# Performance work log

Hardware: AMD Instinct MI355X
Metric: run time of the kernel (lower is better)

## Reference

```python
import jax, jax.numpy as jnp
import numpy as np

B, N, SU, H, NC, NUM_ITER = 1024, 32, 8, 64, 4, 5
E = N * (N - 1)


def _edge_idx(n):
    # Fully-connected graph without self loops; edges grouped contiguously by
    # destination node so that blocks of (n-1) messages sum into one node
    # (matches the original Python segment-sum loop with step = n-1).
    idx = np.arange(n)
    temp_a = np.concatenate([np.delete(idx, j) for j in range(n)])  # sources
    temp_b = np.repeat(idx, n - 1)                                   # destinations
    return temp_a, temp_b


def _lin(x, W, b):
    return x @ W.T + b


def setup_inputs():
    key = jax.random.key(0)
    ks = jax.random.split(key, 20)
    f = jax.random.normal
    return {
        "read_gru": f(ks[0], (B, N, SU), jnp.float32),
        "gru_init": f(ks[1], (B, N, H), jnp.float32),
        "init_features": f(ks[2], (B, N, 3), jnp.float32),
        "edge_weight": f(ks[3], (B, E), jnp.float32),
        "noise_info": jax.random.uniform(ks[4], (B, 1), jnp.float32),
        "x_hat_EP": f(ks[5], (B, N), jnp.float32),
        "variance_EP": jax.random.uniform(ks[6], (B, N), jnp.float32),
        "W1a": f(ks[7], (SU, 3)) * 0.3, "b1a": jnp.zeros((SU,)),
        "W2a": f(ks[8], (H, 2 * SU + 2)) * 0.1, "b2a": jnp.zeros((H,)),
        "W2b": f(ks[9], (H // 2, H)) * 0.1, "b2b": jnp.zeros((H // 2,)),
        "W2c": f(ks[10], (SU, H // 2)) * 0.1, "b2c": jnp.zeros((SU,)),
        "Wih": f(ks[11], (3 * H, SU + 2)) * 0.1, "bih": jnp.zeros((3 * H,)),
        "Whh": f(ks[12], (3 * H, H)) * 0.1, "bhh": jnp.zeros((3 * H,)),
        "W3a": f(ks[13], (H, SU)) * 0.1, "b3a": jnp.zeros((H,)),
        "W3b": f(ks[14], (H // 2, H)) * 0.1, "b3b": jnp.zeros((H // 2,)),
        "W3c": f(ks[15], (NC, H // 2)) * 0.1, "b3c": jnp.zeros((NC,)),
        "W4": f(ks[16], (SU, H)) * 0.1, "b4": jnp.zeros((SU,)),
        "GNN_iter": 0,
    }


def reference(read_gru, gru_init, init_features, edge_weight, noise_info,
              x_hat_EP, variance_EP,
              W1a, b1a, W2a, b2a, W2b, b2b, W2c, b2c,
              Wih, bih, Whh, bhh,
              W3a, b3a, W3b, b3b, W3c, b3c, W4, b4, GNN_iter):
    b, n = init_features.shape[0], init_features.shape[1]
    temp_a, temp_b = _edge_idx(n)
    e = temp_a.shape[0]
    edge_e = edge_weight[:, :, None]                              # [B,E,1]
    noise_e = jnp.broadcast_to(noise_info, (b, e))[:, :, None]    # [B,E,1]
    gru_hidden = gru_init
    for it in range(NUM_ITER):
        if it == 0 and GNN_iter == 0:
            init_nodes = _lin(init_features, W1a, b1a)            # [B,N,SU]
        else:
            init_nodes = read_gru
        s1 = init_nodes[:, temp_a, :]                             # gather sources
        s2 = init_nodes[:, temp_b, :]                             # gather dests
        comb = jnp.concatenate([s1, s2, edge_e, noise_e], axis=2) # [B,E,2SU+2]
        m = jax.nn.relu(_lin(comb, W2a, b2a))
        m = jax.nn.relu(_lin(m, W2b, b2b))
        m = jax.nn.relu(_lin(m, W2c, b2c))                        # [B,E,SU]
        # contiguous blocks of (n-1) messages per destination node
        sum_msgs = m.reshape(b, n, n - 1, -1).sum(axis=2)         # [B,N,SU]
        gin = jnp.concatenate(
            [sum_msgs, x_hat_EP[:, :, None], variance_EP[:, :, None]], axis=2)
        # GRUCell applied per node
        gi = _lin(gin, Wih, bih)
        gh = _lin(gru_hidden, Whh, bhh)
        i_r, i_z, i_n = jnp.split(gi, 3, axis=-1)
        h_r, h_z, h_n = jnp.split(gh, 3, axis=-1)
        r = jax.nn.sigmoid(i_r + h_r)
        z = jax.nn.sigmoid(i_z + h_z)
        cand = jnp.tanh(i_n + r * h_n)
        gru_hidden = (1.0 - z) * cand + z * gru_hidden
        read_gru = _lin(gru_hidden, W4, b4)
    # readout (no activations in original forward)
    p_y_x = _lin(_lin(_lin(read_gru, W3a, b3a), W3b, b3b), W3c, b3c)
    return (p_y_x, read_gru, gru_hidden)
```

## Files before the change

### kernel.cpp

```cpp
#include <hip/hip_runtime.h>
#include <hip/hip_bf16.h>

#define BB 1024
#define NN 32
#define SUD 8
#define HD 64
#define NCD 4
#define ED 992
#define NITER 5

#define O_W2AT 0
#define O_B2A  1152
#define O_W2B  1216
#define O_B2B  3264
#define O_W2CT 3296
#define O_B2C  3552
#define O_WIHT 3560
#define O_BIH  5480
#define O_WHHT 5672
#define O_BHH  17960
#define O_W4T  18152
#define O_B4   18664
#define O_W3AT 18672
#define O_B3A  19184
#define O_W3BT 19248
#define O_B3B  21296
#define O_W3CT 21328
#define O_B3C  21456
#define O_W1AT 21460
#define O_B1A  21484
#define W_TOTAL 21492

#define FRAG_B2_HI  0
#define FRAG_B2_LO  2048
#define FRAG_C      4096
#define FRAG_WHH_HI 4608
#define FRAG_WHH_LO 16896
#define W_EXT (W_TOTAL + 2560 + 12288)

#define GHS 196

typedef const float* fwp;
typedef __attribute__((ext_vector_type(8))) short short8;
typedef __attribute__((ext_vector_type(4))) float float4v;

__device__ __forceinline__ short bf16r(float x) {
  __hip_bfloat16 h = __float2bfloat16(x);
  return __builtin_bit_cast(short, h);
}

__global__ void prep_weights(fwp W2a, fwp b2a, fwp W2b, fwp b2b, fwp W2c, fwp b2c,
                             fwp Wih, fwp bih, fwp Whh, fwp bhh,
                             fwp W3a, fwp b3a, fwp W3b, fwp b3b, fwp W3c, fwp b3c,
                             fwp W4, fwp b4, fwp W1a, fwp b1a, float* __restrict__ ws) {
  int idx = blockIdx.x * 256 + threadIdx.x;
  if (idx >= W_EXT) return;
  if (idx >= W_TOTAL) {
    __hip_bfloat16* wb = (__hip_bfloat16*)(ws + W_TOTAL);
    int e = idx - W_TOTAL;
    if (e < 2048) {
      int j = e & 7, L = (e >> 3) & 63, hs = e >> 9;
      int h = hs >> 1, s = hs & 1;
      float v = W2b[(h * 16 + (L & 15)) * 64 + s * 32 + ((L >> 4) & 3) * 8 + j];
      float hi = __bfloat162float(__float2bfloat16(v));
      wb[FRAG_B2_HI + e] = __float2bfloat16(v);
      wb[FRAG_B2_LO + e] = __float2bfloat16(v - hi);
    } else if (e < 2560) {
      int e2 = e - 2048;
      int j = e2 & 7, L = (e2 >> 3) & 63;
      int su = L & 15, q = L >> 4;
      float v = (su < 8) ? W2c[su * 32 + q * 8 + j] : 0.f;
      wb[FRAG_C + e2] = __float2bfloat16(v);
    } else {
      int e2 = e - 2560;
      int j = e2 & 7, L = (e2 >> 3) & 63, nts = e2 >> 9;
      int nt = nts >> 1, s = nts & 1;
      float v = Whh[(nt * 16 + (L & 15)) * 64 + s * 32 + ((L >> 4) & 3) * 8 + j];
      float hi = __bfloat162float(__float2bfloat16(v));
      wb[FRAG_WHH_HI + e2] = __float2bfloat16(v);
      wb[FRAG_WHH_LO + e2] = __float2bfloat16(v - hi);
    }
    return;
  }
  float v;
  if (idx < O_B2A)       { int p = idx;          int su = p / 64, f = p % 64;   v = W2a[f * 18 + su]; }
  else if (idx < O_W2B)  { v = b2a[idx - O_B2A]; }
  else if (idx < O_B2B)  { v = W2b[idx - O_W2B]; }
  else if (idx < O_W2CT) { v = b2b[idx - O_B2B]; }
  else if (idx < O_B2C)  { int p = idx - O_W2CT; int o = p / 8, su = p % 8;     v = W2c[su * 32 + o]; }
  else if (idx < O_WIHT) { v = b2c[idx - O_B2C]; }
  else if (idx < O_BIH)  { int p = idx - O_WIHT; int k = p / 192, o = p % 192;  v = Wih[o * 10 + k]; }
  else if (idx < O_WHHT) { v = bih[idx - O_BIH]; }
  else if (idx < O_BHH)  { int p = idx - O_WHHT; int k = p / 192, o = p % 192;  v = Whh[o * 64 + k]; }
  else if (idx < O_W4T)  { v = bhh[idx - O_BHH]; }
  else if (idx < O_B4)   { int p = idx - O_W4T;  int k = p / 8, su = p % 8;     v = W4[su * 64 + k]; }
  else if (idx < O_W3AT) { v = b4[idx - O_B4]; }
  else if (idx < O_B3A)  { int p = idx - O_W3AT; int k = p / 64, f = p % 64;    v = W3a[f * 8 + k]; }
  else if (idx < O_W3BT) { v = b3a[idx - O_B3A]; }
  else if (idx < O_B3B)  { int p = idx - O_W3BT; int k = p / 32, f = p % 32;    v = W3b[f * 64 + k]; }
  else if (idx < O_W3CT) { v = b3b[idx - O_B3B]; }
  else if (idx < O_B3C)  { int p = idx - O_W3CT; int k = p / 4, c = p % 4;      v = W3c[c * 32 + k]; }
  else if (idx < O_W1AT) { v = b3c[idx - O_B3C]; }
  else if (idx < O_B1A)  { int p = idx - O_W1AT; int c = p / 8, su = p % 8;     v = W1a[su * 3 + c]; }
  else                   { v = b1a[idx - O_B1A]; }
  ws[idx] = v;
}

#define DO_STEP(KOFF, Y0, Y1, W0, W1, FH0, FH1)                                \
  {                                                                            \
    float4v x0 = *(const float4v*)&sA1[a * 68 + (KOFF)];                       \
    float4v x1 = *(const float4v*)&sA1[a * 68 + (KOFF) + 4];                   \
    float4v z4 = {0.f, 0.f, 0.f, 0.f};                                         \
    float4v t0 = (x0 + Y0) + ewv * W0;                                         \
    float4v t1 = (x1 + Y1) + ewv * W1;                                         \
    t0 = __builtin_elementwise_max(t0, z4);                                    \
    t1 = __builtin_elementwise_max(t1, z4);                                    \
    short8 ahi;                                                                \
    ahi[0] = bf16r(t0.x); ahi[1] = bf16r(t0.y); ahi[2] = bf16r(t0.z);          \
    ahi[3] = bf16r(t0.w); ahi[4] = bf16r(t1.x); ahi[5] = bf16r(t1.y);          \
    ahi[6] = bf16r(t1.z); ahi[7] = bf16r(t1.w);                                \
    accb0 = __builtin_amdgcn_mfma_f32_16x16x32_bf16(ahi, FH0, accb0, 0, 0, 0); \
    accb1 = __builtin_amdgcn_mfma_f32_16x16x32_bf16(ahi, FH1, accb1, 0, 0, 0); \
  }

#define LAUNDER(v) __asm__ __volatile__("" : "+v"(v))

__global__ __launch_bounds__(256, 4) void gnn_fused(
    const float* __restrict__ read_gru_in,
    const float* __restrict__ gru_init,
    const float* __restrict__ feat,
    const float* __restrict__ edge_w,
    const float* __restrict__ noise_in,
    const float* __restrict__ xhat,
    const float* __restrict__ vep,
    const int* __restrict__ gnn_iter_p,
    const float* __restrict__ ws,
    float* __restrict__ out)
{
  __shared__ __attribute__((aligned(16))) char spool[NN * GHS * 4];
  __shared__ __attribute__((aligned(16))) float sH[NN * 68];
  __shared__ float sNodes[NN * 9];
  __shared__ float sSum[NN * 8];
  __shared__ float sEw[ED];
  __shared__ float sC1[64];
  __shared__ float sWew[64];
  __shared__ float sX[NN];
  __shared__ float sV[NN];

  float* const sA1 = (float*)spool;
  float* const sA2 = (float*)(spool + 8704);
  __hip_bfloat16* const sM2 = (__hip_bfloat16*)(spool + 17408);
  float* const sGH = (float*)spool;

  const int b = blockIdx.x;
  const int t = threadIdx.x;
  const int lane = t & 63;
  const int wv = t >> 6;
  const int quad = lane >> 4;
  const int lm = lane & 15;

  const __hip_bfloat16* wb = (const __hip_bfloat16*)(ws + W_TOTAL);

  float noi = noise_in[b];
  for (int e = t; e < ED; e += 256) sEw[e] = edge_w[b * ED + e];
  if (t < NN) { sX[t] = xhat[b * NN + t]; sV[t] = vep[b * NN + t]; }
  if (t < 64) {
    sC1[t]  = ws[O_B2A + t] + noi * ws[O_W2AT + 17 * 64 + t];
    sWew[t] = ws[O_W2AT + 16 * 64 + t];
  }
#pragma unroll
  for (int i = 0; i < 8; ++i) {
    int p = t + 256 * i;
    sH[(p >> 6) * 68 + (p & 63)] = gru_init[b * (NN * HD) + p];
  }
  {
    const int git = gnn_iter_p[0];
    int n = t >> 3, su = t & 7;
    float acc;
    if (git == 0) {
      acc = ws[O_B1A + su];
#pragma unroll
      for (int c = 0; c < 3; ++c)
        acc += ws[O_W1AT + c * 8 + su] * feat[b * (NN * 3) + n * 3 + c];
    } else {
      acc = read_gru_in[b * (NN * SUD) + t];
    }
    sNodes[n * 9 + su] = acc;
  }
  __syncthreads();

  for (int it = 0; it < NITER; ++it) {
    {
      int iva = 0; LAUNDER(iva);
      const float* wsl = ws + iva;
#pragma unroll
      for (int i = 0; i < 8; ++i) {
        int p = t + 256 * i;
        int n = p >> 6, f = p & 63;
        float a1 = 0.f, a2 = 0.f;
#pragma unroll
        for (int su = 0; su < 8; ++su) {
          float nv = sNodes[n * 9 + su];
          a1 += wsl[O_W2AT + su * 64 + f] * nv;
          a2 += wsl[O_W2AT + (8 + su) * 64 + f] * nv;
        }
        sA1[n * 68 + f] = a1;
        sA2[n * 68 + f] = a2 + sC1[iva + f];
      }
    }
    __syncthreads();

    {
      int ive = 0; LAUNDER(ive);
      const float* wsl = ws + ive;
      const __hip_bfloat16* wbl = wb + ive;
      short8 fbh00 = *(const short8*)(wbl + FRAG_B2_HI + (0 * 64 + lane) * 8);
      short8 fbh01 = *(const short8*)(wbl + FRAG_B2_HI + (1 * 64 + lane) * 8);
      short8 fbh10 = *(const short8*)(wbl + FRAG_B2_HI + (2 * 64 + lane) * 8);
      short8 fbh11 = *(const short8*)(wbl + FRAG_B2_HI + (3 * 64 + lane) * 8);
      short8 fcf   = *(const short8*)(wbl + FRAG_C + lane * 8);
      const float b2b0 = wsl[O_B2B + lm];
      const float b2b1 = wsl[O_B2B + 16 + lm];
      const float b2cl = wsl[O_B2C + lm];

      __hip_bfloat16* m2w = sM2 + wv * (16 * 44);
      const int kq0 = quad * 8, kq1 = 32 + quad * 8;
      float4v wwA = *(const float4v*)&sWew[ive + kq0];
      float4v wwB = *(const float4v*)&sWew[ive + kq0 + 4];
      float4v wwC = *(const float4v*)&sWew[ive + kq1];
      float4v wwD = *(const float4v*)&sWew[ive + kq1 + 4];
      for (int ni = 0; ni < 8; ++ni) {
        const int jj = wv * 8 + ni;
        float4v yA = *(const float4v*)&sA2[jj * 68 + kq0];
        float4v yB = *(const float4v*)&sA2[jj * 68 + kq0 + 4];
        float4v yC = *(const float4v*)&sA2[jj * 68 + kq1];
        float4v yD = *(const float4v*)&sA2[jj * 68 + kq1 + 4];
        float psum = 0.f;
#pragma unroll
        for (int tile = 0; tile < 2; ++tile) {
          int kk = tile * 16 + lm;
          int kk2 = (kk < 31) ? kk : 0;
          int a = kk2 + (kk2 >= jj ? 1 : 0);
          float ewv = (kk < 31) ? sEw[ive + jj * 31 + kk] : 0.f;
          float4v accb0 = {0.f, 0.f, 0.f, 0.f};
          float4v accb1 = {0.f, 0.f, 0.f, 0.f};
          DO_STEP(kq0, yA, yB, wwA, wwB, fbh00, fbh10);
          DO_STEP(kq1, yC, yD, wwC, wwD, fbh01, fbh11);
#pragma unroll
          for (int r = 0; r < 4; ++r) {
            float m20 = fmaxf(accb0[r] + b2b0, 0.f);
            float m21 = fmaxf(accb1[r] + b2b1, 0.f);
            m2w[(quad * 4 + r) * 44 + lm]      = __float2bfloat16(m20);
            m2w[(quad * 4 + r) * 44 + 16 + lm] = __float2bfloat16(m21);
          }
          __asm__ __volatile__("" ::: "memory");
          short8 ac = *(const short8*)(m2w + lm * 44 + quad * 8);
          float4v c3 = {0.f, 0.f, 0.f, 0.f};
          c3 = __builtin_amdgcn_mfma_f32_16x16x32_bf16(ac, fcf, c3, 0, 0, 0);
#pragma unroll
          for (int r = 0; r < 4; ++r) {
            float v = fmaxf(c3[r] + b2cl, 0.f);
            if (tile == 1 && r == 3) v = (quad == 3) ? 0.f : v;
            psum += v;
          }
          __asm__ __volatile__("" ::: "memory");
        }
        psum += __shfl_xor(psum, 16);
        psum += __shfl_xor(psum, 32);
        if (lane < 8) sSum[jj * 8 + lane] = psum;
      }
    }
    __syncthreads();

    {
      int ivg = 0; LAUNDER(ivg);
      const __hip_bfloat16* wbl = wb + ivg;
      short8 aH[2][2];
#pragma unroll
      for (int mt = 0; mt < 2; ++mt) {
#pragma unroll
        for (int s = 0; s < 2; ++s) {
          const float* hp = &sH[(mt * 16 + lm) * 68 + s * 32 + quad * 8];
          float4v h0 = *(const float4v*)hp;
          float4v h1 = *(const float4v*)(hp + 4);
          short8 a;
          a[0] = bf16r(h0.x); a[1] = bf16r(h0.y); a[2] = bf16r(h0.z); a[3] = bf16r(h0.w);
          a[4] = bf16r(h1.x); a[5] = bf16r(h1.y); a[6] = bf16r(h1.z); a[7] = bf16r(h1.w);
          aH[mt][s] = a;
        }
      }
#pragma unroll
      for (int nt = 0; nt < 3; ++nt) {
        int gnt = 4 * nt + wv;
        short8 bh0 = *(const short8*)(wbl + FRAG_WHH_HI + ((gnt * 2 + 0) * 64 + lane) * 8);
        short8 bh1 = *(const short8*)(wbl + FRAG_WHH_HI + ((gnt * 2 + 1) * 64 + lane) * 8);
#pragma unroll
        for (int mt = 0; mt < 2; ++mt) {
          float4v acc = {0.f, 0.f, 0.f, 0.f};
          acc = __builtin_amdgcn_mfma_f32_16x16x32_bf16(aH[mt][0], bh0, acc, 0, 0, 0);
          acc = __builtin_amdgcn_mfma_f32_16x16x32_bf16(aH[mt][1], bh1, acc, 0, 0, 0);
#pragma unroll
          for (int r = 0; r < 4; ++r)
            sGH[(mt * 16 + quad * 4 + r) * GHS + gnt * 16 + lm] = acc[r];
        }
      }
    }
    __asm__ __volatile__("" ::: "memory");

    {
      int ivq = 0; LAUNDER(ivq);
      const float* wsl = ws + ivq;
      int lm2 = lane & 15, g = lane >> 4;
      int c = wv * 16 + lm2;
      float ar[8], az[8], inx[8];
      {
        float br  = wsl[O_BIH + c]       + wsl[O_BHH + c];
        float bz  = wsl[O_BIH + 64 + c]  + wsl[O_BHH + 64 + c];
        float bni = wsl[O_BIH + 128 + c];
#pragma unroll
        for (int j = 0; j < 8; ++j) { ar[j] = br; az[j] = bz; inx[j] = bni; }
      }
#pragma unroll
      for (int k = 0; k < 8; ++k) {
        float wr = wsl[O_WIHT + k * 192 + c];
        float wz = wsl[O_WIHT + k * 192 + 64 + c];
        float wn = wsl[O_WIHT + k * 192 + 128 + c];
#pragma unroll
        for (int j = 0; j < 8; ++j) {
          float gg = sSum[(g + 4 * j) * 8 + k];
          ar[j] += wr * gg; az[j] += wz * gg; inx[j] += wn * gg;
        }
      }
      {
        float wr = wsl[O_WIHT + 8 * 192 + c];
        float wz = wsl[O_WIHT + 8 * 192 + 64 + c];
        float wn = wsl[O_WIHT + 8 * 192 + 128 + c];
#pragma unroll
        for (int j = 0; j < 8; ++j) {
          float gg = sX[ivq + g + 4 * j];
          ar[j] += wr * gg; az[j] += wz * gg; inx[j] += wn * gg;
        }
        wr = wsl[O_WIHT + 9 * 192 + c];
        wz = wsl[O_WIHT + 9 * 192 + 64 + c];
        wn = wsl[O_WIHT + 9 * 192 + 128 + c];
#pragma unroll
        for (int j = 0; j < 8; ++j) {
          float gg = sV[ivq + g + 4 * j];
          ar[j] += wr * gg; az[j] += wz * gg; inx[j] += wn * gg;
        }
      }
      float bnh = wsl[O_BHH + 128 + c];
      float hnew[8];
#pragma unroll
      for (int j = 0; j < 8; ++j) {
        int n = g + 4 * j;
        float ghr = sGH[n * GHS + c];
        float ghz = sGH[n * GHS + 64 + c];
        float ghn = sGH[n * GHS + 128 + c] + bnh;
        float r = 1.f / (1.f + __expf(-(ar[j] + ghr)));
        float z = 1.f / (1.f + __expf(-(az[j] + ghz)));
        float cd = inx[j] + r * ghn;
        float e2 = __expf(2.f * cd);
        float th = 1.f - 2.f / (e2 + 1.f);
        hnew[j] = (1.f - z) * th + z * sH[n * 68 + c];
      }
      __syncthreads();
#pragma unroll
      for (int j = 0; j < 8; ++j) sH[(g + 4 * j) * 68 + c] = hnew[j];
    }
    __syncthreads();

    {
      int ivw = 0; LAUNDER(ivw);
      const float* wsl = ws + ivw;
      int n = t >> 3, su = t & 7;
      float c0 = 0.f, c1v = 0.f, c2 = 0.f, c3v = 0.f;
#pragma unroll
      for (int k = 0; k < 64; k += 4) {
        c0  += wsl[O_W4T + (k + 0) * 8 + su] * sH[n * 68 + k + 0];
        c1v += wsl[O_W4T + (k + 1) * 8 + su] * sH[n * 68 + k + 1];
        c2  += wsl[O_W4T + (k + 2) * 8 + su] * sH[n * 68 + k + 2];
        c3v += wsl[O_W4T + (k + 3) * 8 + su] * sH[n * 68 + k + 3];
      }
      sNodes[n * 9 + su] = wsl[O_B4 + su] + ((c0 + c1v) + (c2 + c3v));
    }
    __syncthreads();
  }

#pragma unroll
  for (int i = 0; i < 8; ++i) {
    int p = t + 256 * i;
    int n = p >> 6, f = p & 63;
    float acc = ws[O_B3A + f];
#pragma unroll
    for (int k = 0; k < 8; ++k) acc += ws[O_W3AT + k * 64 + f] * sNodes[n * 9 + k];
    sA1[n * 68 + f] = acc;
  }
  __syncthreads();
#pragma unroll
  for (int i = 0; i < 4; ++i) {
    int p = t + 256 * i;
    int n = p >> 5, f = p & 31;
    float c0 = 0.f, c1v = 0.f, c2 = 0.f, c3v = 0.f;
#pragma unroll
    for (int k = 0; k < 64; k += 4) {
      c0  += ws[O_W3BT + (k + 0) * 32 + f] * sA1[n * 68 + k + 0];
      c1v += ws[O_W3BT + (k + 1) * 32 + f] * sA1[n * 68 + k + 1];
      c2  += ws[O_W3BT + (k + 2) * 32 + f] * sA1[n * 68 + k + 2];
      c3v += ws[O_W3BT + (k + 3) * 32 + f] * sA1[n * 68 + k + 3];
    }
    sA2[n * 33 + f] = ws[O_B3B + f] + ((c0 + c1v) + (c2 + c3v));
  }
  __syncthreads();
  if (t < 128) {
    int n = t >> 2, c = t & 3;
    float acc = ws[O_B3C + c];
#pragma unroll
    for (int k = 0; k < 32; ++k) acc += ws[O_W3CT + k * 4 + c] * sA2[n * 33 + k];
    out[b * (NN * NCD) + t] = acc;
  }
  out[BB * NN * NCD + b * (NN * SUD) + t] = sNodes[(t >> 3) * 9 + (t & 7)];
#pragma unroll
  for (int i = 0; i < 8; ++i) {
    int p = t + 256 * i;
    out[BB * NN * NCD + BB * NN * SUD + b * (NN * HD) + p] =
        sH[(p >> 6) * 68 + (p & 63)];
  }
}

extern "C" void kernel_launch(void* const* d_in, const int* in_sizes, int n_in,
                              void* d_out, int out_size, void* d_ws, size_t ws_size,
                              hipStream_t stream) {
  typedef const float* F32;
  F32 read_gru = (F32)d_in[0];
  F32 gru_init = (F32)d_in[1];
  F32 feat     = (F32)d_in[2];
  F32 edge_w   = (F32)d_in[3];
  F32 noise    = (F32)d_in[4];
  F32 xh       = (F32)d_in[5];
  F32 vp       = (F32)d_in[6];
  F32 W1a = (F32)d_in[7];  F32 b1a = (F32)d_in[8];
  F32 W2a = (F32)d_in[9];  F32 b2a = (F32)d_in[10];
  F32 W2b = (F32)d_in[11]; F32 b2b = (F32)d_in[12];
  F32 W2c = (F32)d_in[13]; F32 b2c = (F32)d_in[14];
  F32 Wih = (F32)d_in[15]; F32 bih = (F32)d_in[16];
  F32 Whh = (F32)d_in[17]; F32 bhh = (F32)d_in[18];
  F32 W3a = (F32)d_in[19]; F32 b3a = (F32)d_in[20];
  F32 W3b = (F32)d_in[21]; F32 b3b = (F32)d_in[22];
  F32 W3c = (F32)d_in[23]; F32 b3c = (F32)d_in[24];
  F32 W4  = (F32)d_in[25]; F32 b4  = (F32)d_in[26];
  const int* git = (const int*)d_in[27];
  float* ws = (float*)d_ws;

  prep_weights<<<(W_EXT + 255) / 256, 256, 0, stream>>>(
      W2a, b2a, W2b, b2b, W2c, b2c, Wih, bih, Whh, bhh,
      W3a, b3a, W3b, b3b, W3c, b3c, W4, b4, W1a, b1a, ws);

  gnn_fused<<<BB, 256, 0, stream>>>(read_gru, gru_init, feat, edge_w, noise,
                                    xh, vp, git, ws, (float*)d_out);
}
```

Baseline: 267.5 us.

## Move node projection to MFMA, hoist fragment loads, pack GRU input math

The per-iteration W2a node projection now runs on bf16 MFMA instead of scalar FMAs, using new pre-swizzled fragments built in prep. The W2b/W2c fragments and biases are hoisted out of the iteration loop, and the unused hi/lo split buffers are dropped. The W2b layout is interleaved so bias loads and message stores can be packed pairs. The GRU input projection uses float2 packed math over a new interleaved Wih copy, and the W4 readout reads raw W4 with float4 vector loads. This trades some precision in the node projection (bf16 inputs) for fewer VALU instructions, and the hoisted fragments raise register pressure.

```diff
diff --git a/kernel.cpp b/kernel.cpp
--- a/kernel.cpp
+++ b/kernel.cpp
@@ -30,23 +30,29 @@
 #define O_W1AT 21460
 #define O_B1A  21484
 #define W_TOTAL 21492
-
-#define FRAG_B2_HI  0
-#define FRAG_B2_LO  2048
-#define FRAG_C      4096
-#define FRAG_WHH_HI 4608
-#define FRAG_WHH_LO 16896
-#define W_EXT (W_TOTAL + 2560 + 12288)
+#define O_WIHP 21492
+#define W_TOTAL2 25332
+
+#define FRAG_B2   0
+#define FRAG_C    2048
+#define FRAG_WHH  2560
+#define FRAG_A2P  14848
+#define FRAG_TOTAL 18944
+#define PREP_TOTAL (W_TOTAL2 + FRAG_TOTAL)
 
 #define GHS 196
 
 typedef const float* fwp;
 typedef __attribute__((ext_vector_type(8))) short short8;
 typedef __attribute__((ext_vector_type(4))) float float4v;
+typedef __attribute__((ext_vector_type(2))) float float2v;
 
 __device__ __forceinline__ short bf16r(float x) {
   __hip_bfloat16 h = __float2bfloat16(x);
   return __builtin_bit_cast(short, h);
+}
+__device__ __forceinline__ float2v mk2(float a, float b) {
+  float2v r; r.x = a; r.y = b; return r;
 }
 
 __global__ void prep_weights(fwp W2a, fwp b2a, fwp W2b, fwp b2b, fwp W2c, fwp b2c,
@@ -54,32 +60,40 @@
                              fwp W3a, fwp b3a, fwp W3b, fwp b3b, fwp W3c, fwp b3c,
                              fwp W4, fwp b4, fwp W1a, fwp b1a, float* __restrict__ ws) {
   int idx = blockIdx.x * 256 + threadIdx.x;
-  if (idx >= W_EXT) return;
-  if (idx >= W_TOTAL) {
-    __hip_bfloat16* wb = (__hip_bfloat16*)(ws + W_TOTAL);
-    int e = idx - W_TOTAL;
+  if (idx >= PREP_TOTAL) return;
+  if (idx >= W_TOTAL2) {
+    __hip_bfloat16* wbw = (__hip_bfloat16*)(ws + W_TOTAL2);
+    int e = idx - W_TOTAL2;
+    float v;
     if (e < 2048) {
       int j = e & 7, L = (e >> 3) & 63, hs = e >> 9;
       int h = hs >> 1, s = hs & 1;
-      float v = W2b[(h * 16 + (L & 15)) * 64 + s * 32 + ((L >> 4) & 3) * 8 + j];
-      float hi = __bfloat162float(__float2bfloat16(v));
-      wb[FRAG_B2_HI + e] = __float2bfloat16(v);
-      wb[FRAG_B2_LO + e] = __float2bfloat16(v - hi);
+      v = W2b[(2 * (L & 15) + h) * 64 + s * 32 + ((L >> 4) & 3) * 8 + j];
     } else if (e < 2560) {
       int e2 = e - 2048;
       int j = e2 & 7, L = (e2 >> 3) & 63;
       int su = L & 15, q = L >> 4;
-      float v = (su < 8) ? W2c[su * 32 + q * 8 + j] : 0.f;
-      wb[FRAG_C + e2] = __float2bfloat16(v);
-    } else {
+      v = (su < 8) ? W2c[su * 32 + q * 8 + j] : 0.f;
+    } else if (e < 14848) {
       int e2 = e - 2560;
       int j = e2 & 7, L = (e2 >> 3) & 63, nts = e2 >> 9;
       int nt = nts >> 1, s = nts & 1;
-      float v = Whh[(nt * 16 + (L & 15)) * 64 + s * 32 + ((L >> 4) & 3) * 8 + j];
-      float hi = __bfloat162float(__float2bfloat16(v));
-      wb[FRAG_WHH_HI + e2] = __float2bfloat16(v);
-      wb[FRAG_WHH_LO + e2] = __float2bfloat16(v - hi);
-    }
+      v = Whh[(nt * 16 + (L & 15)) * 64 + s * 32 + ((L >> 4) & 3) * 8 + j];
+    } else {
+      int e2 = e - 14848;
+      int j = e2 & 7, L = (e2 >> 3) & 63, nt = e2 >> 9;
+      int col = L & 15, kq = L >> 4;
+      v = 0.f;
+      if (kq == 0) v = (nt < 4) ? W2a[(nt * 16 + col) * 18 + j]
+                                : W2a[((nt - 4) * 16 + col) * 18 + 8 + j];
+    }
+    wbw[e] = __float2bfloat16(v);
+    return;
+  }
+  if (idx >= W_TOTAL) {
+    int p = idx - O_WIHP;
+    int o = p / 20, k = (p % 20) >> 1;
+    ws[idx] = Wih[o * 10 + k];
     return;
   }
   float v;
@@ -135,11 +149,12 @@
     const float* __restrict__ vep,
     const int* __restrict__ gnn_iter_p,
     const float* __restrict__ ws,
+    const float* __restrict__ W4g,
     float* __restrict__ out)
 {
   __shared__ __attribute__((aligned(16))) char spool[NN * GHS * 4];
   __shared__ __attribute__((aligned(16))) float sH[NN * 68];
-  __shared__ float sNodes[NN * 9];
+  __shared__ __attribute__((aligned(16))) float sNodes[NN * 10];
   __shared__ float sSum[NN * 8];
   __shared__ float sEw[ED];
   __shared__ float sC1[64];
@@ -159,7 +174,7 @@
   const int quad = lane >> 4;
   const int lm = lane & 15;
 
-  const __hip_bfloat16* wb = (const __hip_bfloat16*)(ws + W_TOTAL);
+  const __hip_bfloat16* wb = (const __hip_bfloat16*)(ws + W_TOTAL2);
 
   float noi = noise_in[b];
   for (int e = t; e < ED; e += 256) sEw[e] = edge_w[b * ED + e];
@@ -185,44 +200,57 @@
     } else {
       acc = read_gru_in[b * (NN * SUD) + t];
     }
-    sNodes[n * 9 + su] = acc;
-  }
+    sNodes[n * 10 + su] = acc;
+  }
+
+  short8 fbh00 = *(const short8*)(wb + FRAG_B2 + (0 * 64 + lane) * 8);
+  short8 fbh01 = *(const short8*)(wb + FRAG_B2 + (1 * 64 + lane) * 8);
+  short8 fbh10 = *(const short8*)(wb + FRAG_B2 + (2 * 64 + lane) * 8);
+  short8 fbh11 = *(const short8*)(wb + FRAG_B2 + (3 * 64 + lane) * 8);
+  short8 fcf   = *(const short8*)(wb + FRAG_C + lane * 8);
+  float2v b2bv = *(const float2v*)&ws[O_B2B + 2 * lm];
+  float   b2cl = ws[O_B2C + lm];
+
   __syncthreads();
 
   for (int it = 0; it < NITER; ++it) {
     {
       int iva = 0; LAUNDER(iva);
-      const float* wsl = ws + iva;
-#pragma unroll
-      for (int i = 0; i < 8; ++i) {
-        int p = t + 256 * i;
-        int n = p >> 6, f = p & 63;
-        float a1 = 0.f, a2 = 0.f;
-#pragma unroll
-        for (int su = 0; su < 8; ++su) {
-          float nv = sNodes[n * 9 + su];
-          a1 += wsl[O_W2AT + su * 64 + f] * nv;
-          a2 += wsl[O_W2AT + (8 + su) * 64 + f] * nv;
-        }
-        sA1[n * 68 + f] = a1;
-        sA2[n * 68 + f] = a2 + sC1[iva + f];
+      const __hip_bfloat16* fp = wb + FRAG_A2P + iva;
+      short8 aN[2];
+#pragma unroll
+      for (int mt = 0; mt < 2; ++mt) {
+        short8 a = {0, 0, 0, 0, 0, 0, 0, 0};
+        if (quad == 0) {
+          float4v n0 = *(const float4v*)&sNodes[(mt * 16 + lm) * 10];
+          float4v n1 = *(const float4v*)&sNodes[(mt * 16 + lm) * 10 + 4];
+          a[0] = bf16r(n0.x); a[1] = bf16r(n0.y); a[2] = bf16r(n0.z); a[3] = bf16r(n0.w);
+          a[4] = bf16r(n1.x); a[5] = bf16r(n1.y); a[6] = bf16r(n1.z); a[7] = bf16r(n1.w);
+        }
+        aN[mt] = a;
+      }
+      const int f = wv * 16 + lm;
+      const float c1f = sC1[f];
+#pragma unroll
+      for (int half = 0; half < 2; ++half) {
+        short8 bfr = *(const short8*)(fp + ((half * 4 + wv) * 64 + lane) * 8);
+#pragma unroll
+        for (int mt = 0; mt < 2; ++mt) {
+          float4v acc = {0.f, 0.f, 0.f, 0.f};
+          acc = __builtin_amdgcn_mfma_f32_16x16x32_bf16(aN[mt], bfr, acc, 0, 0, 0);
+#pragma unroll
+          for (int r = 0; r < 4; ++r) {
+            int node = mt * 16 + quad * 4 + r;
+            if (half == 0) sA1[node * 68 + f] = acc[r];
+            else           sA2[node * 68 + f] = acc[r] + c1f;
+          }
+        }
       }
     }
     __syncthreads();
 
     {
       int ive = 0; LAUNDER(ive);
-      const float* wsl = ws + ive;
-      const __hip_bfloat16* wbl = wb + ive;
-      short8 fbh00 = *(const short8*)(wbl + FRAG_B2_HI + (0 * 64 + lane) * 8);
-      short8 fbh01 = *(const short8*)(wbl + FRAG_B2_HI + (1 * 64 + lane) * 8);
-      short8 fbh10 = *(const short8*)(wbl + FRAG_B2_HI + (2 * 64 + lane) * 8);
-      short8 fbh11 = *(const short8*)(wbl + FRAG_B2_HI + (3 * 64 + lane) * 8);
-      short8 fcf   = *(const short8*)(wbl + FRAG_C + lane * 8);
-      const float b2b0 = wsl[O_B2B + lm];
-      const float b2b1 = wsl[O_B2B + 16 + lm];
-      const float b2cl = wsl[O_B2C + lm];
-
       __hip_bfloat16* m2w = sM2 + wv * (16 * 44);
       const int kq0 = quad * 8, kq1 = 32 + quad * 8;
       float4v wwA = *(const float4v*)&sWew[ive + kq0];
@@ -248,10 +276,12 @@
           DO_STEP(kq1, yC, yD, wwC, wwD, fbh01, fbh11);
 #pragma unroll
           for (int r = 0; r < 4; ++r) {
-            float m20 = fmaxf(accb0[r] + b2b0, 0.f);
-            float m21 = fmaxf(accb1[r] + b2b1, 0.f);
-            m2w[(quad * 4 + r) * 44 + lm]      = __float2bfloat16(m20);
-            m2w[(quad * 4 + r) * 44 + 16 + lm] = __float2bfloat16(m21);
+            float m20 = fmaxf(accb0[r] + b2bv.x, 0.f);
+            float m21 = fmaxf(accb1[r] + b2bv.y, 0.f);
+            ushort2 pp;
+            pp.x = (unsigned short)bf16r(m20);
+            pp.y = (unsigned short)bf16r(m21);
+            *(ushort2*)(m2w + (quad * 4 + r) * 44 + 2 * lm) = pp;
           }
           __asm__ __volatile__("" ::: "memory");
           short8 ac = *(const short8*)(m2w + lm * 44 + quad * 8);
@@ -292,8 +322,8 @@
 #pragma unroll
       for (int nt = 0; nt < 3; ++nt) {
         int gnt = 4 * nt + wv;
-        short8 bh0 = *(const short8*)(wbl + FRAG_WHH_HI + ((gnt * 2 + 0) * 64 + lane) * 8);
-        short8 bh1 = *(const short8*)(wbl + FRAG_WHH_HI + ((gnt * 2 + 1) * 64 + lane) * 8);
+        short8 bh0 = *(const short8*)(wbl + FRAG_WHH + ((gnt * 2 + 0) * 64 + lane) * 8);
+        short8 bh1 = *(const short8*)(wbl + FRAG_WHH + ((gnt * 2 + 1) * 64 + lane) * 8);
 #pragma unroll
         for (int mt = 0; mt < 2; ++mt) {
           float4v acc = {0.f, 0.f, 0.f, 0.f};
@@ -312,41 +342,29 @@
       const float* wsl = ws + ivq;
       int lm2 = lane & 15, g = lane >> 4;
       int c = wv * 16 + lm2;
-      float ar[8], az[8], inx[8];
-      {
-        float br  = wsl[O_BIH + c]       + wsl[O_BHH + c];
-        float bz  = wsl[O_BIH + 64 + c]  + wsl[O_BHH + 64 + c];
-        float bni = wsl[O_BIH + 128 + c];
-#pragma unroll
-        for (int j = 0; j < 8; ++j) { ar[j] = br; az[j] = bz; inx[j] = bni; }
-      }
-#pragma unroll
-      for (int k = 0; k < 8; ++k) {
-        float wr = wsl[O_WIHT + k * 192 + c];
-        float wz = wsl[O_WIHT + k * 192 + 64 + c];
-        float wn = wsl[O_WIHT + k * 192 + 128 + c];
-#pragma unroll
-        for (int j = 0; j < 8; ++j) {
-          float gg = sSum[(g + 4 * j) * 8 + k];
-          ar[j] += wr * gg; az[j] += wz * gg; inx[j] += wn * gg;
-        }
-      }
-      {
-        float wr = wsl[O_WIHT + 8 * 192 + c];
-        float wz = wsl[O_WIHT + 8 * 192 + 64 + c];
-        float wn = wsl[O_WIHT + 8 * 192 + 128 + c];
-#pragma unroll
-        for (int j = 0; j < 8; ++j) {
-          float gg = sX[ivq + g + 4 * j];
-          ar[j] += wr * gg; az[j] += wz * gg; inx[j] += wn * gg;
-        }
-        wr = wsl[O_WIHT + 9 * 192 + c];
-        wz = wsl[O_WIHT + 9 * 192 + 64 + c];
-        wn = wsl[O_WIHT + 9 * 192 + 128 + c];
-#pragma unroll
-        for (int j = 0; j < 8; ++j) {
-          float gg = sV[ivq + g + 4 * j];
-          ar[j] += wr * gg; az[j] += wz * gg; inx[j] += wn * gg;
+      const float* wih = wsl + O_WIHP;
+      float br = wsl[O_BIH + c]       + wsl[O_BHH + c];
+      float bz = wsl[O_BIH + 64 + c]  + wsl[O_BHH + 64 + c];
+      float bn = wsl[O_BIH + 128 + c];
+      float2v ar2[4], az2[4], an2[4];
+#pragma unroll
+      for (int jp = 0; jp < 4; ++jp) {
+        ar2[jp] = mk2(br, br); az2[jp] = mk2(bz, bz); an2[jp] = mk2(bn, bn);
+      }
+#pragma unroll
+      for (int k = 0; k < 10; ++k) {
+        float2v wr = *(const float2v*)&wih[(c) * 20 + 2 * k];
+        float2v wz = *(const float2v*)&wih[(64 + c) * 20 + 2 * k];
+        float2v wn = *(const float2v*)&wih[(128 + c) * 20 + 2 * k];
+#pragma unroll
+        for (int jp = 0; jp < 4; ++jp) {
+          float2v gg;
+          if (k < 8)       gg = mk2(sSum[(g + 8 * jp) * 8 + k], sSum[(g + 8 * jp + 4) * 8 + k]);
+          else if (k == 8) gg = mk2(sX[g + 8 * jp], sX[g + 8 * jp + 4]);
+          else             gg = mk2(sV[g + 8 * jp], sV[g + 8 * jp + 4]);
+          ar2[jp] += wr * gg;
+          az2[jp] += wz * gg;
+          an2[jp] += wn * gg;
         }
       }
       float bnh = wsl[O_BHH + 128 + c];
@@ -354,12 +372,16 @@
 #pragma unroll
       for (int j = 0; j < 8; ++j) {
         int n = g + 4 * j;
+        int jp = j >> 1;
+        float arj = (j & 1) ? ar2[jp].y : ar2[jp].x;
+        float azj = (j & 1) ? az2[jp].y : az2[jp].x;
+        float anj = (j & 1) ? an2[jp].y : an2[jp].x;
         float ghr = sGH[n * GHS + c];
         float ghz = sGH[n * GHS + 64 + c];
         float ghn = sGH[n * GHS + 128 + c] + bnh;
-        float r = 1.f / (1.f + __expf(-(ar[j] + ghr)));
-        float z = 1.f / (1.f + __expf(-(az[j] + ghz)));
-        float cd = inx[j] + r * ghn;
+        float r = 1.f / (1.f + __expf(-(arj + ghr)));
+        float z = 1.f / (1.f + __expf(-(azj + ghz)));
+        float cd = anj + r * ghn;
         float e2 = __expf(2.f * cd);
         float th = 1.f - 2.f / (e2 + 1.f);
         hnew[j] = (1.f - z) * th + z * sH[n * 68 + c];
@@ -372,17 +394,16 @@
 
     {
       int ivw = 0; LAUNDER(ivw);
-      const float* wsl = ws + ivw;
       int n = t >> 3, su = t & 7;
-      float c0 = 0.f, c1v = 0.f, c2 = 0.f, c3v = 0.f;
+      const float* w4r = W4g + ivw + su * 64;
+      float4v acc4 = {0.f, 0.f, 0.f, 0.f};
 #pragma unroll
       for (int k = 0; k < 64; k += 4) {
-        c0  += wsl[O_W4T + (k + 0) * 8 + su] * sH[n * 68 + k + 0];
-        c1v += wsl[O_W4T + (k + 1) * 8 + su] * sH[n * 68 + k + 1];
-        c2  += wsl[O_W4T + (k + 2) * 8 + su] * sH[n * 68 + k + 2];
-        c3v += wsl[O_W4T + (k + 3) * 8 + su] * sH[n * 68 + k + 3];
-      }
-      sNodes[n * 9 + su] = wsl[O_B4 + su] + ((c0 + c1v) + (c2 + c3v));
+        float4v w = *(const float4v*)&w4r[k];
+        float4v h = *(const float4v*)&sH[n * 68 + k];
+        acc4 += w * h;
+      }
+      sNodes[n * 10 + su] = ws[O_B4 + su] + ((acc4.x + acc4.y) + (acc4.z + acc4.w));
     }
     __syncthreads();
   }
@@ -393,7 +414,7 @@
     int n = p >> 6, f = p & 63;
     float acc = ws[O_B3A + f];
 #pragma unroll
-    for (int k = 0; k < 8; ++k) acc += ws[O_W3AT + k * 64 + f] * sNodes[n * 9 + k];
+    for (int k = 0; k < 8; ++k) acc += ws[O_W3AT + k * 64 + f] * sNodes[n * 10 + k];
     sA1[n * 68 + f] = acc;
   }
   __syncthreads();
@@ -419,7 +440,7 @@
     for (int k = 0; k < 32; ++k) acc += ws[O_W3CT + k * 4 + c] * sA2[n * 33 + k];
     out[b * (NN * NCD) + t] = acc;
   }
-  out[BB * NN * NCD + b * (NN * SUD) + t] = sNodes[(t >> 3) * 9 + (t & 7)];
+  out[BB * NN * NCD + b * (NN * SUD) + t] = sNodes[(t >> 3) * 10 + (t & 7)];
 #pragma unroll
   for (int i = 0; i < 8; ++i) {
     int p = t + 256 * i;
@@ -452,10 +473,10 @@
   const int* git = (const int*)d_in[27];
   float* ws = (float*)d_ws;
 
-  prep_weights<<<(W_EXT + 255) / 256, 256, 0, stream>>>(
+  prep_weights<<<(PREP_TOTAL + 255) / 256, 256, 0, stream>>>(
       W2a, b2a, W2b, b2b, W2c, b2c, Wih, bih, Whh, bhh,
       W3a, b3a, W3b, b3b, W3c, b3c, W4, b4, W1a, b1a, ws);
 
   gnn_fused<<<BB, 256, 0, stream>>>(read_gru, gru_init, feat, edge_w, noise,
-                                    xh, vp, git, ws, (float*)d_out);
+                                    xh, vp, git, ws, W4, (float*)d_out);
 }
```

After: 277.5 us. 3.7% more time.
